# Kernel tuning notes

Hardware: AMD Instinct MI355X
Metric: run time of the kernel (lower is better)

## Reference

```python
import jax, jax.numpy as jnp
import numpy as np
import math

B, S, E, H, FF = 2, 2048, 1024, 16, 4096
HD = E // H
EPS = 1e-6


def layer_norm(x, gamma, beta):
    mu = jnp.mean(x, axis=-1, keepdims=True)
    var = jnp.mean(jnp.square(x - mu), axis=-1, keepdims=True)
    return (x - mu) * jax.lax.rsqrt(var + EPS) * gamma + beta


def setup_inputs() -> dict:
    key = jax.random.key(0)
    ks = jax.random.split(key, 8)
    x_embeds = jax.random.normal(ks[0], (B, S, E), dtype=jnp.float32)
    # causal mask: True means masked (j > i), broadcastable over batch/heads
    mask = jnp.triu(jnp.ones((S, S), dtype=bool), k=1)[None, None]
    sc = 1.0 / math.sqrt(E)
    w_kqv = jax.random.normal(ks[1], (3 * E, E), dtype=jnp.float32) * sc
    w_o = jax.random.normal(ks[2], (E, E), dtype=jnp.float32) * sc
    w_up = jax.random.normal(ks[3], (FF, E), dtype=jnp.float32) * sc
    b_up = jnp.zeros((FF,), dtype=jnp.float32)
    w_down = jax.random.normal(ks[4], (E, FF), dtype=jnp.float32) / math.sqrt(FF)
    b_down = jnp.zeros((E,), dtype=jnp.float32)
    g1 = jnp.ones((E,), dtype=jnp.float32)
    b1 = jnp.zeros((E,), dtype=jnp.float32)
    g2 = jnp.ones((E,), dtype=jnp.float32)
    b2 = jnp.zeros((E,), dtype=jnp.float32)
    return {"x_embeds": x_embeds, "mask": mask, "w_kqv": w_kqv, "w_o": w_o,
            "w_up": w_up, "b_up": b_up, "w_down": w_down, "b_down": b_down,
            "g1": g1, "b1": b1, "g2": g2, "b2": b2}


def reference(x_embeds, mask, w_kqv, w_o, w_up, b_up, w_down, b_down, g1, b1, g2, b2):
    b, s = x_embeds.shape[0], x_embeds.shape[1]
    # --- attention ---
    kqv = x_embeds @ w_kqv.T                      # [B,S,3E]
    kqv = kqv.reshape(b, s, 3, H, HD).transpose(0, 3, 2, 1, 4)  # [B,H,3,S,HD]
    xk, xq, xv = kqv[:, :, 0], kqv[:, :, 1], kqv[:, :, 2]
    attn = jnp.einsum('bhqd,bhkd->bhqk', xq, xk) / math.sqrt(HD)
    attn = jnp.where(mask, -jnp.inf, attn)
    attn = jax.nn.softmax(attn, axis=-1)
    out = jnp.einsum('bhqk,bhkd->bhqd', attn, xv)  # [B,H,S,HD]
    out = out.transpose(0, 2, 1, 3).reshape(b, s, E)
    out = out @ w_o.T
    x = layer_norm(out + x_embeds, g1, b1)
    # --- ffnn ---
    h = jax.nn.relu(x @ w_up.T + b_up)
    h = h @ w_down.T + b_down
    return layer_norm(h + x, g2, b2)
```

## Files before the change

kernel.cpp:

```cpp
#include <hip/hip_runtime.h>
#include <stdint.h>

#define B_ 2
#define S_ 2048
#define E_ 1024
#define H_ 16
#define HD_ 64
#define FF_ 4096
#define M_ 4096
#define LOG2E_ 1.44269504f

typedef short bf16x8 __attribute__((ext_vector_type(8)));
typedef float f32x4  __attribute__((ext_vector_type(4)));
typedef short shortx4 __attribute__((ext_vector_type(4)));

#define MFMA16(a,b,c) __builtin_amdgcn_mfma_f32_16x16x32_bf16(a,b,c,0,0,0)

__device__ __forceinline__ short f2bf(float f) {
  uint32_t u = __builtin_bit_cast(uint32_t, f);
  u += 0x7fffu + ((u >> 16) & 1u);
  return (short)(u >> 16);
}
__device__ __forceinline__ float bf2f(short b) {
  uint32_t u = ((uint32_t)(uint16_t)b) << 16;
  return __builtin_bit_cast(float, u);
}
__device__ __forceinline__ float exp2_hw(float x) {
  float r;
  asm("v_exp_f32 %0, %1" : "=v"(r) : "v"(x));
  return r;
}

template<int CTRL>
__device__ __forceinline__ float dpp_ror(float x) {
  return __builtin_bit_cast(float,
    __builtin_amdgcn_update_dpp(0, __builtin_bit_cast(int, x), CTRL, 0xF, 0xF, true));
}
__device__ __forceinline__ float dpp_max16(float v) {
  v = fmaxf(v, dpp_ror<0x128>(v));
  v = fmaxf(v, dpp_ror<0x124>(v));
  v = fmaxf(v, dpp_ror<0x122>(v));
  v = fmaxf(v, dpp_ror<0x121>(v));
  return v;
}
__device__ __forceinline__ float dpp_sum16(float v) {
  v += dpp_ror<0x128>(v);
  v += dpp_ror<0x124>(v);
  v += dpp_ror<0x122>(v);
  v += dpp_ror<0x121>(v);
  return v;
}

#define GLDS16(g, l) __builtin_amdgcn_global_load_lds( \
    (const __attribute__((address_space(1))) unsigned int*)(g), \
    (__attribute__((address_space(3))) unsigned int*)(l), 16, 0, 0)

__global__ void cast_all(const float* __restrict__ x, const float* __restrict__ wkqv,
                         const float* __restrict__ wo, const float* __restrict__ wup,
                         const float* __restrict__ wdown,
                         short* __restrict__ xb, short* __restrict__ wkqvb,
                         short* __restrict__ wob, short* __restrict__ wupb,
                         short* __restrict__ wdownb) {
  const int stride = gridDim.x * blockDim.x;
  for (int i = blockIdx.x * blockDim.x + threadIdx.x; i < 4194304; i += stride) {
    const int e = i << 2;
    const float* src; short* dst; int off;
    if (e < 4194304)       { src = x;     dst = xb;     off = e; }
    else if (e < 7340032)  { src = wkqv;  dst = wkqvb;  off = e - 4194304; }
    else if (e < 8388608)  { src = wo;    dst = wob;    off = e - 7340032; }
    else if (e < 12582912) { src = wup;   dst = wupb;   off = e - 8388608; }
    else                   { src = wdown; dst = wdownb; off = e - 12582912; }
    float4 v = *(const float4*)(src + off);
    shortx4 o;
    o.x = f2bf(v.x); o.y = f2bf(v.y); o.z = f2bf(v.z); o.w = f2bf(v.w);
    *(shortx4*)(dst + off) = o;
  }
}

template<int BN, int SK, int EPI, typename OutT>
__global__ __launch_bounds__(512, 2) void gemm256_bt(
    const short* __restrict__ A, const short* __restrict__ Bw,
    OutT* __restrict__ C0, OutT* __restrict__ C1,
    OutT* __restrict__ C2, OutT* __restrict__ C3,
    const float* __restrict__ bias,
    int M, int N, int K)
{
  constexpr int WCN  = BN / 4;
  constexpr int NJ   = WCN / 16;
  constexpr int NJH  = NJ / 2;
  constexpr int ISSB = BN / 64;

  __shared__ short Al[2][256 * 64];
  __shared__ short Bl[2][BN * 64];
  const int tid = threadIdx.x;
  const int w = tid >> 6, lane = tid & 63;
  const int lr = lane & 15, lg = lane >> 4;
  const int ntiles = N / BN;
  const int nwg = gridDim.x;
  const int bid = blockIdx.x;
  const int swz = (bid & 7) * (nwg >> 3) + (bid >> 3);
  const int tn = swz % ntiles, tm = swz / ntiles;
  const int m0 = tm << 8, n0 = tn * BN;
  const int wrm = (w >> 2) << 7;
  const int wcn = (w & 3) * WCN;

  const int kper = K / SK;
  const int kbeg = (SK > 1) ? (int)blockIdx.y * kper : 0;
  const int T = kper >> 6;
  OutT* __restrict__ C = C0;
  if constexpr (SK > 1) {
    const int sl = blockIdx.y;
    C = (sl == 0) ? C0 : (sl == 1) ? C1 : (sl == 2) ? C2 : C3;
  }

  const int srow = lane >> 3;
  const int scol = ((lane & 7) ^ srow) << 3;
  const short* Ag[4]; const short* Bg[ISSB];
  #pragma unroll
  for (int i = 0; i < 4; ++i)
    Ag[i] = A + (size_t)(m0 + (w + i * 8) * 8 + srow) * K + kbeg + scol;
  #pragma unroll
  for (int i = 0; i < ISSB; ++i)
    Bg[i] = Bw + (size_t)(n0 + (w + i * 8) * 8 + srow) * K + kbeg + scol;

  f32x4 acc[8][NJ] = {};

  #pragma unroll
  for (int i = 0; i < 4; ++i) GLDS16(Ag[i], &Al[0][(w + i * 8) * 512]);
  #pragma unroll
  for (int i = 0; i < ISSB; ++i) GLDS16(Bg[i], &Bl[0][(w + i * 8) * 512]);

  for (int t = 0; t < T; ++t) {
    const int buf = t & 1;
    const bool more = (t + 1 < T);
    const int k1 = (t + 1) << 6;

    bf16x8 af[8], bfLo[NJH * 2], bfHi[NJH * 2];
    const int ph0 = lg ^ (lr & 7);
    const int ph1 = (4 + lg) ^ (lr & 7);

    if (more) {
      #pragma unroll
      for (int i = 0; i < 4; ++i) GLDS16(Ag[i] + k1, &Al[buf ^ 1][(w + i * 8) * 512]);
      #pragma unroll
      for (int i = 0; i < ISSB; ++i) GLDS16(Bg[i] + k1, &Bl[buf ^ 1][(w + i * 8) * 512]);
      if constexpr (ISSB == 4) asm volatile("s_waitcnt vmcnt(8)" ::: "memory");
      else                     asm volatile("s_waitcnt vmcnt(6)" ::: "memory");
    } else {
      asm volatile("s_waitcnt vmcnt(0)" ::: "memory");
    }
    __builtin_amdgcn_sched_barrier(0);
    __builtin_amdgcn_s_barrier();

    #pragma unroll
    for (int i = 0; i < 4; ++i) {
      const int R = wrm + i * 16 + lr;
      af[i * 2]     = *(const bf16x8*)&Al[buf][R * 64 + ph0 * 8];
      af[i * 2 + 1] = *(const bf16x8*)&Al[buf][R * 64 + ph1 * 8];
    }
    #pragma unroll
    for (int j = 0; j < NJH; ++j) {
      const int R = wcn + j * 16 + lr;
      bfLo[j * 2]     = *(const bf16x8*)&Bl[buf][R * 64 + ph0 * 8];
      bfLo[j * 2 + 1] = *(const bf16x8*)&Bl[buf][R * 64 + ph1 * 8];
    }
    __builtin_amdgcn_s_setprio(1);
    #pragma unroll
    for (int i = 0; i < 4; ++i)
      #pragma unroll
      for (int j = 0; j < NJH; ++j) {
        acc[i][j] = MFMA16(af[i * 2],     bfLo[j * 2],     acc[i][j]);
        acc[i][j] = MFMA16(af[i * 2 + 1], bfLo[j * 2 + 1], acc[i][j]);
      }
    __builtin_amdgcn_s_setprio(0);

    #pragma unroll
    for (int j = 0; j < NJH; ++j) {
      const int R = wcn + (j + NJH) * 16 + lr;
      bfHi[j * 2]     = *(const bf16x8*)&Bl[buf][R * 64 + ph0 * 8];
      bfHi[j * 2 + 1] = *(const bf16x8*)&Bl[buf][R * 64 + ph1 * 8];
    }
    __builtin_amdgcn_s_setprio(1);
    #pragma unroll
    for (int i = 0; i < 4; ++i)
      #pragma unroll
      for (int j = 0; j < NJH; ++j) {
        acc[i][j + NJH] = MFMA16(af[i * 2],     bfHi[j * 2],     acc[i][j + NJH]);
        acc[i][j + NJH] = MFMA16(af[i * 2 + 1], bfHi[j * 2 + 1], acc[i][j + NJH]);
      }
    __builtin_amdgcn_s_setprio(0);

    #pragma unroll
    for (int i = 0; i < 4; ++i) {
      const int R = wrm + (i + 4) * 16 + lr;
      af[i * 2]     = *(const bf16x8*)&Al[buf][R * 64 + ph0 * 8];
      af[i * 2 + 1] = *(const bf16x8*)&Al[buf][R * 64 + ph1 * 8];
    }
    __builtin_amdgcn_s_setprio(1);
    #pragma unroll
    for (int i = 0; i < 4; ++i)
      #pragma unroll
      for (int j = 0; j < NJH; ++j) {
        acc[i + 4][j + NJH] = MFMA16(af[i * 2],     bfHi[j * 2],     acc[i + 4][j + NJH]);
        acc[i + 4][j + NJH] = MFMA16(af[i * 2 + 1], bfHi[j * 2 + 1], acc[i + 4][j + NJH]);
      }
    #pragma unroll
    for (int i = 0; i < 4; ++i)
      #pragma unroll
      for (int j = 0; j < NJH; ++j) {
        acc[i + 4][j] = MFMA16(af[i * 2],     bfLo[j * 2],     acc[i + 4][j]);
        acc[i + 4][j] = MFMA16(af[i * 2 + 1], bfLo[j * 2 + 1], acc[i + 4][j]);
      }
    __builtin_amdgcn_s_setprio(0);

    __builtin_amdgcn_s_barrier();
  }

  #pragma unroll
  for (int j = 0; j < NJ; ++j) {
    const int col = n0 + wcn + j * 16 + lr;
    float bv = 0.f;
    if constexpr (EPI == 1) bv = bias[col];
    #pragma unroll
    for (int i = 0; i < 8; ++i) {
      #pragma unroll
      for (int r = 0; r < 4; ++r) {
        const int row = m0 + wrm + i * 16 + lg * 4 + r;
        float v = acc[i][j][r] + bv;
        if constexpr (EPI == 1) v = fmaxf(v, 0.f);
        if constexpr (sizeof(OutT) == 2) C[(size_t)row * N + col] = f2bf(v);
        else                             C[(size_t)row * N + col] = v;
      }
    }
  }
}

template<int SK, int EPI, typename OutT>
__global__ __launch_bounds__(256) void gemm_bt(
    const short* __restrict__ A, const short* __restrict__ Bw,
    OutT* __restrict__ C0, OutT* __restrict__ C1, const float* __restrict__ bias,
    int M, int N, int K)
{
  __shared__ short Al[2][128 * 32];
  __shared__ short Bl[2][128 * 32];
  const int tid  = threadIdx.x;
  const int w    = tid >> 6, lane = tid & 63;
  const int ntiles = N >> 7;
  const int nwg = gridDim.x;
  const int bid = blockIdx.x;
  const int swz = (bid & 7) * (nwg >> 3) + (bid >> 3);
  const int tn = swz % ntiles, tm = swz / ntiles;
  const int m0 = tm << 7, n0 = tn << 7;
  const int wr = (w >> 1) << 6, wc = (w & 1) << 6;
  const int lr = lane & 15, lk = (lane >> 4) << 3;
  const int ra = lane >> 2, colA = (lane & 3) << 3;

  const int kper = K / SK;
  const int kbeg = (SK > 1) ? (int)blockIdx.y * kper : 0;
  const int T = kper >> 5;
  OutT* __restrict__ C = (SK > 1 && blockIdx.y) ? C1 : C0;

  const short* Ag0 = A  + (size_t)(m0 + w * 16 + ra) * K + colA;
  const short* Ag1 = A  + (size_t)(m0 + (w + 4) * 16 + ra) * K + colA;
  const short* Bg0 = Bw + (size_t)(n0 + w * 16 + ra) * K + colA;
  const short* Bg1 = Bw + (size_t)(n0 + (w + 4) * 16 + ra) * K + colA;

  f32x4 acc[4][4] = {};

  {
    const int k0 = kbeg;
    GLDS16(Ag0 + k0, &Al[0][w * 512]);
    GLDS16(Ag1 + k0, &Al[0][(w + 4) * 512]);
    GLDS16(Bg0 + k0, &Bl[0][w * 512]);
    GLDS16(Bg1 + k0, &Bl[0][(w + 4) * 512]);
  }

  for (int it = 0; it < T; ++it) {
    const int buf = it & 1;
    if (it + 1 < T) {
      const int k1 = kbeg + ((it + 1) << 5);
      GLDS16(Ag0 + k1, &Al[buf ^ 1][w * 512]);
      GLDS16(Ag1 + k1, &Al[buf ^ 1][(w + 4) * 512]);
      GLDS16(Bg0 + k1, &Bl[buf ^ 1][w * 512]);
      GLDS16(Bg1 + k1, &Bl[buf ^ 1][(w + 4) * 512]);
      asm volatile("s_waitcnt vmcnt(4)" ::: "memory");
    } else {
      asm volatile("s_waitcnt vmcnt(0)" ::: "memory");
    }
    __builtin_amdgcn_sched_barrier(0);
    __builtin_amdgcn_s_barrier();

    bf16x8 af[4], bfr[4];
    #pragma unroll
    for (int i = 0; i < 4; ++i)
      af[i] = *(const bf16x8*)&Al[buf][(wr + i * 16 + lr) * 32 + lk];
    #pragma unroll
    for (int j = 0; j < 4; ++j)
      bfr[j] = *(const bf16x8*)&Bl[buf][(wc + j * 16 + lr) * 32 + lk];
    #pragma unroll
    for (int i = 0; i < 4; ++i)
      #pragma unroll
      for (int j = 0; j < 4; ++j)
        acc[i][j] = MFMA16(af[i], bfr[j], acc[i][j]);

    __builtin_amdgcn_s_barrier();
  }

  const int lg = lane >> 4;
  #pragma unroll
  for (int j = 0; j < 4; ++j) {
    const int col = n0 + wc + j * 16 + lr;
    float bv = 0.f;
    if constexpr (SK == 1 && EPI != 0) bv = bias[col];
    #pragma unroll
    for (int i = 0; i < 4; ++i) {
      #pragma unroll
      for (int r = 0; r < 4; ++r) {
        const int row = m0 + wr + i * 16 + lg * 4 + r;
        float v = acc[i][j][r] + bv;
        if constexpr (SK == 1 && EPI == 1) v = fmaxf(v, 0.f);
        if constexpr (sizeof(OutT) == 2) C[(size_t)row * N + col] = f2bf(v);
        else                             C[(size_t)row * N + col] = v;
      }
    }
  }
}

__global__ __launch_bounds__(512) void attn_kernel(
    const short* __restrict__ kqv, short* __restrict__ out)
{
  __shared__ short Kt[2][64][72];
  __shared__ short Vt[2][64][72];
  __shared__ short Pl[8][16][64];

  const int tid = threadIdx.x, w = tid >> 6, lane = tid & 63;
  const int wt = w & 3;
  const int p = blockIdx.x;
  const int bh = blockIdx.y;
  const int b = bh >> 4, h = bh & 15;
  const int q0 = ((w < 4) ? (31 - p) : p) << 6;
  const int nkb = 32 - p;
  const int lr = lane & 15, lg = lane >> 4;

  const size_t rowq = (size_t)(b * S_ + q0 + wt * 16 + lr) * 3072 + 1024 + h * 64;
  bf16x8 qf[2];
  qf[0] = *(const bf16x8*)&kqv[rowq + lg * 8];
  qf[1] = *(const bf16x8*)&kqv[rowq + 32 + lg * 8];
  #pragma unroll
  for (int ks = 0; ks < 2; ++ks)
    #pragma unroll
    for (int e = 0; e < 8; ++e)
      qf[ks][e] = f2bf(bf2f(qf[ks][e]) * 0.125f);

  f32x4 acc[4] = {};
  float m_run[4], l_run[4];
  #pragma unroll
  for (int r = 0; r < 4; ++r) { m_run[r] = -1e30f; l_run[r] = 0.f; }

  const int skk = tid >> 3;
  const int sc  = (tid & 7) << 3;
  const int vws = (tid & 7) << 3;
  const int vkc = skk ^ vws;
  const short* gstage = kqv + (size_t)b * S_ * 3072 + h * 64 + sc;

  {
    bf16x8 kreg = *(const bf16x8*)&gstage[(size_t)skk * 3072];
    bf16x8 vreg = *(const bf16x8*)&gstage[(size_t)skk * 3072 + 2048];
    *(bf16x8*)&Kt[0][skk][sc] = kreg;
    #pragma unroll
    for (int e = 0; e < 8; ++e) Vt[0][sc + e][vkc] = vreg[e];
  }
  __syncthreads();

  for (int kbi = 0; kbi < nkb; ++kbi) {
    const int buf = kbi & 1;
    const int kb = kbi << 6;

    bf16x8 kreg, vreg;
    const bool more = (kbi + 1 < nkb);
    if (more) {
      const size_t gb = (size_t)(((kbi + 1) << 6) + skk) * 3072;
      kreg = *(const bf16x8*)&gstage[gb];
      vreg = *(const bf16x8*)&gstage[gb + 2048];
    }

    if (kb <= q0 + wt * 16 + 15) {
      f32x4 sacc[4] = {};
      __builtin_amdgcn_s_setprio(1);
      #pragma unroll
      for (int jt = 0; jt < 4; ++jt) {
        #pragma unroll
        for (int ks = 0; ks < 2; ++ks) {
          bf16x8 kf = *(const bf16x8*)&Kt[buf][jt * 16 + lr][ks * 32 + lg * 8];
          sacc[jt] = MFMA16(qf[ks], kf, sacc[jt]);
        }
      }
      __builtin_amdgcn_s_setprio(0);
      const bool full = (kb + 63 <= q0 + wt * 16);
      float rmax[4];
      if (full) {
        #pragma unroll
        for (int r = 0; r < 4; ++r)
          rmax[r] = fmaxf(fmaxf(sacc[0][r], sacc[1][r]), fmaxf(sacc[2][r], sacc[3][r]));
      } else {
        #pragma unroll
        for (int r = 0; r < 4; ++r) rmax[r] = -1e30f;
        #pragma unroll
        for (int jt = 0; jt < 4; ++jt) {
          const int kpos = kb + jt * 16 + lr;
          #pragma unroll
          for (int r = 0; r < 4; ++r) {
            const int qrow = q0 + wt * 16 + lg * 4 + r;
            float v = (kpos <= qrow) ? sacc[jt][r] : -1e30f;
            sacc[jt][r] = v;
            rmax[r] = fmaxf(rmax[r], v);
          }
        }
      }
      #pragma unroll
      for (int r = 0; r < 4; ++r) rmax[r] = dpp_max16(rmax[r]);
      int need = 0;
      #pragma unroll
      for (int r = 0; r < 4; ++r) need |= (rmax[r] > m_run[r] + 8.f) ? 1 : 0;
      if (__any(need)) {
        #pragma unroll
        for (int r = 0; r < 4; ++r) {
          const float mn = fmaxf(m_run[r], rmax[r]);
          const float al = exp2_hw((m_run[r] - mn) * LOG2E_);
          m_run[r] = mn;
          l_run[r] *= al;
          #pragma unroll
          for (int dt = 0; dt < 4; ++dt) acc[dt][r] *= al;
        }
      }
      float m2[4], rsum[4];
      #pragma unroll
      for (int r = 0; r < 4; ++r) { m2[r] = m_run[r] * LOG2E_; rsum[r] = 0.f; }
      #pragma unroll
      for (int jt = 0; jt < 4; ++jt)
        #pragma unroll
        for (int r = 0; r < 4; ++r) {
          const float pv = exp2_hw(__builtin_fmaf(sacc[jt][r], LOG2E_, -m2[r]));
          sacc[jt][r] = pv;
          rsum[r] += pv;
        }
      #pragma unroll
      for (int r = 0; r < 4; ++r) { rsum[r] = dpp_sum16(rsum[r]); l_run[r] += rsum[r]; }
      #pragma unroll
      for (int jt = 0; jt < 4; ++jt) {
        uint32_t w01, w23;
        asm("v_cvt_pk_bf16_f32 %0, %1, %2" : "=v"(w01) : "v"(sacc[jt][0]), "v"(sacc[jt][1]));
        asm("v_cvt_pk_bf16_f32 %0, %1, %2" : "=v"(w23) : "v"(sacc[jt][2]), "v"(sacc[jt][3]));
        const int slot = jt * 2 + (lr >> 3);
        const int el = lr & 7;
        #pragma unroll
        for (int r = 0; r < 4; ++r) {
          const int row = lg * 4 + r;
          const uint32_t word = (r < 2) ? w01 : w23;
          const short val = (short)((r & 1) ? (word >> 16) : (word & 0xffffu));
          Pl[w][row][((slot ^ (row & 7)) << 3) + el] = val;
        }
      }
      bf16x8 pa[2];
      pa[0] = *(const bf16x8*)&Pl[w][lr][((0 * 4 + lg) ^ (lr & 7)) << 3];
      pa[1] = *(const bf16x8*)&Pl[w][lr][((1 * 4 + lg) ^ (lr & 7)) << 3];
      __builtin_amdgcn_s_setprio(1);
      #pragma unroll
      for (int dt = 0; dt < 4; ++dt) {
        const int vswz = (2 * dt + (lr >> 3)) << 3;
        #pragma unroll
        for (int ks = 0; ks < 2; ++ks) {
          bf16x8 vb = *(const bf16x8*)&Vt[buf][dt * 16 + lr][(ks * 32 + lg * 8) ^ vswz];
          acc[dt] = MFMA16(pa[ks], vb, acc[dt]);
        }
      }
      __builtin_amdgcn_s_setprio(0);
    }

    if (more) {
      *(bf16x8*)&Kt[buf ^ 1][skk][sc] = kreg;
      #pragma unroll
      for (int e = 0; e < 8; ++e) Vt[buf ^ 1][sc + e][vkc] = vreg[e];
    }
    __syncthreads();
  }

  #pragma unroll
  for (int dt = 0; dt < 4; ++dt) {
    #pragma unroll
    for (int r = 0; r < 4; ++r) {
      const int d = h * 64 + dt * 16 + lr;
      const int q_row = q0 + wt * 16 + lg * 4 + r;
      out[(size_t)(b * S_ + q_row) * E_ + d] = f2bf(acc[dt][r] / l_run[r]);
    }
  }
}

__global__ __launch_bounds__(256) void ln_fold2(
    const short* __restrict__ y0, const short* __restrict__ y1,
    const float* __restrict__ res,
    const float* __restrict__ gam, const float* __restrict__ bet,
    short* __restrict__ outp)
{
  const int row = blockIdx.x, tid = threadIdx.x, lane = tid & 63, w = tid >> 6;
  const size_t base = (size_t)row * E_;
  shortx4 a0 = ((const shortx4*)(y0 + base))[tid];
  shortx4 a1 = ((const shortx4*)(y1 + base))[tid];
  float4 rv = ((const float4*)(res + base))[tid];
  float r[4];
  r[0] = bf2f(a0.x) + bf2f(a1.x) + rv.x;
  r[1] = bf2f(a0.y) + bf2f(a1.y) + rv.y;
  r[2] = bf2f(a0.z) + bf2f(a1.z) + rv.z;
  r[3] = bf2f(a0.w) + bf2f(a1.w) + rv.w;
  float s  = r[0] + r[1] + r[2] + r[3];
  float ss = r[0]*r[0] + r[1]*r[1] + r[2]*r[2] + r[3]*r[3];
  #pragma unroll
  for (int m = 32; m >= 1; m >>= 1) { s += __shfl_xor(s, m); ss += __shfl_xor(ss, m); }
  __shared__ float red[8];
  if (lane == 0) { red[w] = s; red[4 + w] = ss; }
  __syncthreads();
  s  = red[0] + red[1] + red[2] + red[3];
  ss = red[4] + red[5] + red[6] + red[7];
  const float mu  = s * (1.f / E_);
  const float var = ss * (1.f / E_) - mu * mu;
  const float rs  = rsqrtf(var + 1e-6f);
  float4 gv = ((const float4*)gam)[tid];
  float4 bv = ((const float4*)bet)[tid];
  shortx4 o;
  o.x = f2bf((r[0] - mu) * rs * gv.x + bv.x);
  o.y = f2bf((r[1] - mu) * rs * gv.y + bv.y);
  o.z = f2bf((r[2] - mu) * rs * gv.z + bv.z);
  o.w = f2bf((r[3] - mu) * rs * gv.w + bv.w);
  ((shortx4*)(outp + base))[tid] = o;
}

__global__ __launch_bounds__(256) void ln_fold4(
    const short* __restrict__ y0, const short* __restrict__ y1,
    const short* __restrict__ y2, const short* __restrict__ y3,
    const float* __restrict__ bias, const short* __restrict__ res,
    const float* __restrict__ gam, const float* __restrict__ bet,
    float* __restrict__ outp)
{
  const int row = blockIdx.x, tid = threadIdx.x, lane = tid & 63, w = tid >> 6;
  const size_t base = (size_t)row * E_;
  shortx4 a0 = ((const shortx4*)(y0 + base))[tid];
  shortx4 a1 = ((const shortx4*)(y1 + base))[tid];
  shortx4 a2 = ((const shortx4*)(y2 + base))[tid];
  shortx4 a3 = ((const shortx4*)(y3 + base))[tid];
  shortx4 rb = ((const shortx4*)(res + base))[tid];
  float4 bi = ((const float4*)bias)[tid];
  float r[4];
  #pragma unroll
  for (int j = 0; j < 4; ++j)
    r[j] = bf2f(a0[j]) + bf2f(a1[j]) + bf2f(a2[j]) + bf2f(a3[j]) + bf2f(rb[j]);
  r[0] += bi.x; r[1] += bi.y; r[2] += bi.z; r[3] += bi.w;
  float s  = r[0] + r[1] + r[2] + r[3];
  float ss = r[0]*r[0] + r[1]*r[1] + r[2]*r[2] + r[3]*r[3];
  #pragma unroll
  for (int m = 32; m >= 1; m >>= 1) { s += __shfl_xor(s, m); ss += __shfl_xor(ss, m); }
  __shared__ float red[8];
  if (lane == 0) { red[w] = s; red[4 + w] = ss; }
  __syncthreads();
  s  = red[0] + red[1] + red[2] + red[3];
  ss = red[4] + red[5] + red[6] + red[7];
  const float mu  = s * (1.f / E_);
  const float var = ss * (1.f / E_) - mu * mu;
  const float rs  = rsqrtf(var + 1e-6f);
  float4 gv = ((const float4*)gam)[tid];
  float4 bv = ((const float4*)bet)[tid];
  float4 o;
  o.x = (r[0] - mu) * rs * gv.x + bv.x;
  o.y = (r[1] - mu) * rs * gv.y + bv.y;
  o.z = (r[2] - mu) * rs * gv.z + bv.z;
  o.w = (r[3] - mu) * rs * gv.w + bv.w;
  ((float4*)(outp + base))[tid] = o;
}

extern "C" void kernel_launch(void* const* d_in, const int* in_sizes, int n_in,
                              void* d_out, int out_size, void* d_ws, size_t ws_size,
                              hipStream_t stream) {
  const float* x      = (const float*)d_in[0];
  const float* w_kqv  = (const float*)d_in[2];
  const float* w_o    = (const float*)d_in[3];
  const float* w_up   = (const float*)d_in[4];
  const float* b_up   = (const float*)d_in[5];
  const float* w_down = (const float*)d_in[6];
  const float* b_down = (const float*)d_in[7];
  const float* g1     = (const float*)d_in[8];
  const float* b1     = (const float*)d_in[9];
  const float* g2     = (const float*)d_in[10];
  const float* b2     = (const float*)d_in[11];
  float* out = (float*)d_out;

  char* ws = (char*)d_ws;
  short* xb     = (short*)(ws);
  short* wkqvb  = (short*)(ws + ((size_t)8  << 20));
  short* wob    = (short*)(ws + ((size_t)14 << 20));
  short* wupb   = (short*)(ws + ((size_t)16 << 20));
  short* wdownb = (short*)(ws + ((size_t)24 << 20));
  short* kqv    = (short*)(ws + ((size_t)32 << 20));
  short* proj0b = (short*)(ws + ((size_t)32 << 20));
  short* proj1b = (short*)(ws + ((size_t)40 << 20));
  short* hbuf   = (short*)(ws + ((size_t)32 << 20));
  short* attno  = (short*)(ws + ((size_t)64 << 20));
  short* xln    = (short*)(ws + ((size_t)72 << 20));
  short* dwn0   = (short*)(ws);
  short* dwn1   = (short*)(ws + ((size_t)8  << 20));
  short* dwn2   = (short*)(ws + ((size_t)16 << 20));
  short* dwn3   = (short*)(ws + ((size_t)64 << 20));

  cast_all<<<2048, 256, 0, stream>>>(x, w_kqv, w_o, w_up, w_down,
                                     xb, wkqvb, wob, wupb, wdownb);

  gemm_bt<1, 0, short><<<24 * 32, 256, 0, stream>>>(xb, wkqvb, kqv, nullptr, nullptr, M_, 3 * E_, E_);
  attn_kernel<<<dim3(16, B_ * H_), 512, 0, stream>>>(kqv, attno);
  gemm256_bt<128, 2, 0, short><<<dim3(128, 2), 512, 0, stream>>>(
      attno, wob, proj0b, proj1b, nullptr, nullptr, nullptr, M_, E_, E_);
  ln_fold2<<<M_, 256, 0, stream>>>(proj0b, proj1b, x, g1, b1, xln);
  gemm256_bt<256, 1, 1, short><<<256, 512, 0, stream>>>(
      xln, wupb, hbuf, nullptr, nullptr, nullptr, b_up, M_, FF_, E_);
  gemm256_bt<256, 4, 0, short><<<dim3(64, 4), 512, 0, stream>>>(
      hbuf, wdownb, dwn0, dwn1, dwn2, dwn3, nullptr, M_, E_, FF_);
  ln_fold4<<<M_, 256, 0, stream>>>(dwn0, dwn1, dwn2, dwn3, b_down, xln, g2, b2, out);
}
```

Before: 224.8 us.

## Split attention KV range across two blocks and merge partials with separate kernel

Adds a grid z-dimension so each query block processes half of its causal key range. Each half writes unnormalized fp32 outputs plus running max and sum, and a new merge kernel combines them with rescaling into bf16. This doubles the attention grid to improve CU occupancy and balance, at the cost of extra fp32 partial traffic and an additional kernel launch. Workspace buffers are re-laid out to fit the partials.

```diff
diff --git a/kernel.cpp b/kernel.cpp
--- a/kernel.cpp
+++ b/kernel.cpp
@@ -327,7 +327,9 @@
 }
 
 __global__ __launch_bounds__(512) void attn_kernel(
-    const short* __restrict__ kqv, short* __restrict__ out)
+    const short* __restrict__ kqv,
+    float* __restrict__ o0, float* __restrict__ o1,
+    float2* __restrict__ mlbuf)
 {
   __shared__ short Kt[2][64][72];
   __shared__ short Vt[2][64][72];
@@ -337,9 +339,13 @@
   const int wt = w & 3;
   const int p = blockIdx.x;
   const int bh = blockIdx.y;
+  const int s = blockIdx.z;
   const int b = bh >> 4, h = bh & 15;
   const int q0 = ((w < 4) ? (31 - p) : p) << 6;
   const int nkb = 32 - p;
+  const int halfk = (nkb + 1) >> 1;
+  const int t0 = s ? halfk : 0;
+  const int t1 = s ? nkb : halfk;
   const int lr = lane & 15, lg = lane >> 4;
 
   const size_t rowq = (size_t)(b * S_ + q0 + wt * 16 + lr) * 3072 + 1024 + h * 64;
@@ -364,20 +370,21 @@
   const short* gstage = kqv + (size_t)b * S_ * 3072 + h * 64 + sc;
 
   {
-    bf16x8 kreg = *(const bf16x8*)&gstage[(size_t)skk * 3072];
-    bf16x8 vreg = *(const bf16x8*)&gstage[(size_t)skk * 3072 + 2048];
+    const size_t gb = (size_t)((t0 << 6) + skk) * 3072;
+    bf16x8 kreg = *(const bf16x8*)&gstage[gb];
+    bf16x8 vreg = *(const bf16x8*)&gstage[gb + 2048];
     *(bf16x8*)&Kt[0][skk][sc] = kreg;
     #pragma unroll
     for (int e = 0; e < 8; ++e) Vt[0][sc + e][vkc] = vreg[e];
   }
   __syncthreads();
 
-  for (int kbi = 0; kbi < nkb; ++kbi) {
-    const int buf = kbi & 1;
+  for (int kbi = t0; kbi < t1; ++kbi) {
+    const int buf = (kbi - t0) & 1;
     const int kb = kbi << 6;
 
     bf16x8 kreg, vreg;
-    const bool more = (kbi + 1 < nkb);
+    const bool more = (kbi + 1 < t1);
     if (more) {
       const size_t gb = (size_t)(((kbi + 1) << 6) + skk) * 3072;
       kreg = *(const bf16x8*)&gstage[gb];
@@ -485,15 +492,49 @@
     __syncthreads();
   }
 
+  float* __restrict__ opart = s ? o1 : o0;
   #pragma unroll
   for (int dt = 0; dt < 4; ++dt) {
     #pragma unroll
     for (int r = 0; r < 4; ++r) {
       const int d = h * 64 + dt * 16 + lr;
       const int q_row = q0 + wt * 16 + lg * 4 + r;
-      out[(size_t)(b * S_ + q_row) * E_ + d] = f2bf(acc[dt][r] / l_run[r]);
-    }
-  }
+      opart[(size_t)(b * S_ + q_row) * E_ + d] = acc[dt][r];
+    }
+  }
+  if (lr == 0) {
+    #pragma unroll
+    for (int r = 0; r < 4; ++r) {
+      const int q_row = q0 + wt * 16 + lg * 4 + r;
+      float2 v; v.x = m_run[r]; v.y = l_run[r];
+      mlbuf[(((size_t)s * 32 + bh) << 11) + q_row] = v;
+    }
+  }
+}
+
+__global__ __launch_bounds__(256) void merge_attn(
+    const float* __restrict__ o0, const float* __restrict__ o1,
+    const float2* __restrict__ mlbuf, short* __restrict__ attno)
+{
+  const int row = blockIdx.x, tid = threadIdx.x;
+  const int b = row >> 11, q = row & 2047;
+  const int h = (tid * 4) >> 6;
+  const size_t bh = (size_t)b * 16 + h;
+  const float2 A = mlbuf[(bh << 11) + q];
+  const float2 Bp = mlbuf[((32 + bh) << 11) + q];
+  const float m = fmaxf(A.x, Bp.x);
+  const float sA = exp2_hw((A.x - m) * LOG2E_);
+  const float sB = exp2_hw((Bp.x - m) * LOG2E_);
+  const float inv = 1.f / (A.y * sA + Bp.y * sB);
+  const size_t base = (size_t)row * E_;
+  float4 va = ((const float4*)(o0 + base))[tid];
+  float4 vb = ((const float4*)(o1 + base))[tid];
+  shortx4 o;
+  o.x = f2bf((va.x * sA + vb.x * sB) * inv);
+  o.y = f2bf((va.y * sA + vb.y * sB) * inv);
+  o.z = f2bf((va.z * sA + vb.z * sB) * inv);
+  o.w = f2bf((va.w * sA + vb.w * sB) * inv);
+  ((shortx4*)(attno + base))[tid] = o;
 }
 
 __global__ __launch_bounds__(256) void ln_fold2(
@@ -599,11 +640,14 @@
   short* wupb   = (short*)(ws + ((size_t)16 << 20));
   short* wdownb = (short*)(ws + ((size_t)24 << 20));
   short* kqv    = (short*)(ws + ((size_t)32 << 20));
+  float* opart0 = (float*)(ws + ((size_t)64 << 20));
+  float* opart1 = (float*)(ws + ((size_t)80 << 20));
+  float2* mlbuf = (float2*)(ws + ((size_t)56 << 20));
+  short* attno  = (short*)(ws);
   short* proj0b = (short*)(ws + ((size_t)32 << 20));
   short* proj1b = (short*)(ws + ((size_t)40 << 20));
+  short* xln    = (short*)(ws + ((size_t)88 << 20));
   short* hbuf   = (short*)(ws + ((size_t)32 << 20));
-  short* attno  = (short*)(ws + ((size_t)64 << 20));
-  short* xln    = (short*)(ws + ((size_t)72 << 20));
   short* dwn0   = (short*)(ws);
   short* dwn1   = (short*)(ws + ((size_t)8  << 20));
   short* dwn2   = (short*)(ws + ((size_t)16 << 20));
@@ -613,7 +657,8 @@
                                      xb, wkqvb, wob, wupb, wdownb);
 
   gemm_bt<1, 0, short><<<24 * 32, 256, 0, stream>>>(xb, wkqvb, kqv, nullptr, nullptr, M_, 3 * E_, E_);
-  attn_kernel<<<dim3(16, B_ * H_), 512, 0, stream>>>(kqv, attno);
+  attn_kernel<<<dim3(16, B_ * H_, 2), 512, 0, stream>>>(kqv, opart0, opart1, mlbuf);
+  merge_attn<<<M_, 256, 0, stream>>>(opart0, opart1, mlbuf, attno);
   gemm256_bt<128, 2, 0, short><<<dim3(128, 2), 512, 0, stream>>>(
       attno, wob, proj0b, proj1b, nullptr, nullptr, nullptr, M_, E_, E_);
   ln_fold2<<<M_, 256, 0, stream>>>(proj0b, proj1b, x, g1, b1, xln);
```

Measured after the change: 239.3 us. +6.4%, slower.
